# Kernel tuning notes

Measured on AMD Instinct MI355X. Metric: run time of the kernel, lower is better.

The kernel has to match this reference:

```python
import jax, jax.numpy as jnp
import numpy as np

B, N, CQ, CH, H = 2, 2048, 256, 256, 8
D = CH // H  # head_dim = 32


def setup_inputs() -> dict:
    key = jax.random.key(0)
    ks = jax.random.split(key, 10)
    s = 0.02
    return {
        "q_x": jax.random.normal(ks[0], (B, N, CQ), dtype=jnp.float32),
        "attn_bias": jax.random.normal(ks[1], (B, H, N, N), dtype=jnp.float32),
        "Wq": jax.random.normal(ks[2], (CQ, CH), dtype=jnp.float32) * s,
        "bq": jnp.zeros((CH,), dtype=jnp.float32),
        "Wk": jax.random.normal(ks[3], (CQ, CH), dtype=jnp.float32) * s,
        "Wv": jax.random.normal(ks[4], (CQ, CH), dtype=jnp.float32) * s,
        "Wout": jax.random.normal(ks[5], (CH, CQ), dtype=jnp.float32) * s,
        "bout": jnp.zeros((CQ,), dtype=jnp.float32),
        "Wg": jax.random.normal(ks[6], (CQ, CQ), dtype=jnp.float32) * s,
        "bg": jnp.zeros((CQ,), dtype=jnp.float32),
        "gbias": jnp.ones((CQ,), dtype=jnp.float32),
    }


def reference(q_x, attn_bias, Wq, bq, Wk, Wv, Wout, bout, Wg, bg, gbias):
    # prep_qkv: project, split heads; scale q by 1/sqrt(head_dim) (apply_scale path)
    scale = 1.0 / jnp.sqrt(jnp.asarray(D, q_x.dtype))
    q = ((q_x @ Wq + bq).reshape(B, N, H, D)) * scale  # [B,N,H,D]
    k = (q_x @ Wk).reshape(B, N, H, D)
    v = (q_x @ Wv).reshape(B, N, H, D)
    # attention with additive pair bias
    scores = jnp.einsum("bqhd,bkhd->bhqk", q, k) + attn_bias  # [B,H,N,N]
    attn = jax.nn.softmax(scores, axis=-1)
    o = jnp.einsum("bhqk,bkhd->bqhd", attn, v).reshape(B, N, CH)  # merge heads
    # wrap_up: output projection + sigmoid gate (gating_bias init ones)
    out = o @ Wout + bout  # [B,N,CQ]
    gate = jax.nn.sigmoid(q_x @ Wg + bg + gbias)
    return gate * out
```

## Files before the change

kernel.cpp:

```cpp
#include <hip/hip_runtime.h>

#define BB 2
#define NN 2048
#define CQc 256
#define CHc 256
#define HHc 8
#define DDc 32

typedef __bf16 bf16_t;
typedef bf16_t bf16x8 __attribute__((ext_vector_type(8)));
typedef float f32x4 __attribute__((ext_vector_type(4)));

#define LOG2E 1.4426950408889634f

static __device__ __forceinline__ unsigned short f2bf(float f) {
  union { float f; unsigned u; } a; a.f = f;
  unsigned r = a.u + 0x7FFFu + ((a.u >> 16) & 1u);
  return (unsigned short)(r >> 16);
}

static __device__ __forceinline__ bf16x8 ldb8(const unsigned short* p) {
  return *reinterpret_cast<const bf16x8*>(p);
}

__global__ void prep_w(const float* __restrict__ Wq, const float* __restrict__ Wk,
                       const float* __restrict__ Wv, const float* __restrict__ Wg,
                       const float* __restrict__ Wo, unsigned short* __restrict__ wt) {
  int gid = blockIdx.x * 256 + threadIdx.x;
  int w = gid >> 16, r = gid & 65535;
  int n = r >> 8, k = r & 255;
  const float* W = (w == 0) ? Wq : (w == 1) ? Wk : (w == 2) ? Wv : (w == 3) ? Wg : Wo;
  wt[gid] = f2bf(W[k * 256 + n]);
}

__global__ __launch_bounds__(256) void proj_k(
    const float* __restrict__ X, const float* __restrict__ bq,
    const float* __restrict__ bg, const float* __restrict__ gbias,
    const unsigned short* __restrict__ wt,
    unsigned short* __restrict__ q_ws, unsigned short* __restrict__ k_ws,
    unsigned short* __restrict__ vt_ws, float* __restrict__ gate_ws) {
  const int tid = threadIdx.x;
  const int wave = tid >> 6, l = tid & 63, g = l >> 4, l15 = l & 15;
  const int mrow = blockIdx.x * 64 + wave * 16 + l15;
  const int c0 = blockIdx.y * 64;
  const int widx = c0 >> 8;
  const int nin0 = c0 & 255;
  const unsigned short* W = wt + widx * 65536;

  f32x4 acc[4];
#pragma unroll
  for (int st = 0; st < 4; ++st) acc[st] = f32x4{0.f, 0.f, 0.f, 0.f};

#pragma unroll
  for (int kk0 = 0; kk0 < 256; kk0 += 32) {
    const float* xp = X + mrow * 256 + kk0 + 8 * g;
    f32x4 x0 = *reinterpret_cast<const f32x4*>(xp);
    f32x4 x1 = *reinterpret_cast<const f32x4*>(xp + 4);
    union { unsigned short u[8]; bf16x8 v; } av;
#pragma unroll
    for (int e = 0; e < 4; ++e) { av.u[e] = f2bf(x0[e]); av.u[4 + e] = f2bf(x1[e]); }
#pragma unroll
    for (int st = 0; st < 4; ++st) {
      bf16x8 bv = ldb8(W + (nin0 + st * 16 + l15) * 256 + kk0 + 8 * g);
      acc[st] = __builtin_amdgcn_mfma_f32_16x16x32_bf16(av.v, bv, acc[st], 0, 0, 0);
    }
  }

  const int mb = blockIdx.x * 64 + wave * 16 + 4 * g;
#pragma unroll
  for (int st = 0; st < 4; ++st) {
    const int n = nin0 + st * 16 + l15;
#pragma unroll
    for (int j = 0; j < 4; ++j) {
      const int m = mb + j;
      const int b = m >> 11, t = m & 2047;
      float val = acc[st][j];
      if (widx == 0) {
        int h = n >> 5, d = n & 31;
        q_ws[((b * 8 + h) * 2048 + t) * 32 + d] =
            f2bf((val + bq[n]) * (0.17677669529663687f * LOG2E));
      } else if (widx == 1) {
        int h = n >> 5, d = n & 31;
        k_ws[((b * 8 + h) * 2048 + t) * 32 + d] = f2bf(val);
      } else if (widx == 2) {
        int h = n >> 5, d = n & 31;
        vt_ws[((b * 8 + h) * 32 + d) * 2048 + t] = f2bf(val);
      } else {
        float z = val + bg[n] + gbias[n];
        gate_ws[m * 256 + n] = 1.0f / (1.0f + __expf(-z));
      }
    }
  }
}

__global__ __launch_bounds__(256) void attn_k(
    const unsigned short* __restrict__ q_ws, const unsigned short* __restrict__ k_ws,
    const unsigned short* __restrict__ vt_ws, const float* __restrict__ bias,
    unsigned short* __restrict__ o_ws) {
  __shared__ float sbias[4 * 3 * 1024];
  __shared__ unsigned short plds[4 * 16 * 72];
  const int tid = threadIdx.x;
  const int wave = tid >> 6, l = tid & 63, g = l >> 4, l15 = l & 15;
  const int bh = blockIdx.x >> 5, qt = blockIdx.x & 31;
  const int qr0 = qt * 64 + wave * 16;
  const int kvbase = bh * 2048;
  unsigned short* pw = plds + wave * (16 * 72);
  float* sb = sbias + wave * 3072;

  const bf16x8 qa = ldb8(q_ws + (size_t)(kvbase + qr0 + l15) * 32 + 8 * g);
  const unsigned short* kbase = k_ws + (size_t)kvbase * 32 + 8 * g + l15 * 32;
  const unsigned short* vbase = vt_ws + (size_t)(bh * 32 + l15) * 2048 + 8 * g;
  const float* bsrc = bias + ((size_t)bh << 22) + (size_t)(qr0 + (l >> 4)) * 2048 + (l & 15) * 4;

  auto stage = [&](int bidx, int k0) {
    float* dst = sb + bidx * 1024;
#pragma unroll
    for (int qq = 0; qq < 4; ++qq)
      __builtin_amdgcn_global_load_lds(
          (const __attribute__((address_space(1))) void*)(bsrc + (size_t)qq * 8192 + k0),
          (__attribute__((address_space(3))) void*)(dst + qq * 256), 16, 0, 0);
  };

  float mr[4], lr[4];
  f32x4 oacc[2];
#pragma unroll
  for (int j = 0; j < 4; ++j) { mr[j] = -1e30f; lr[j] = 0.0f; }
  oacc[0] = f32x4{0.f, 0.f, 0.f, 0.f};
  oacc[1] = f32x4{0.f, 0.f, 0.f, 0.f};

  stage(0, 0);
  stage(1, 64);
  int cb = 0;
#pragma unroll 1
  for (int kt = 0; kt < 32; ++kt) {
    const int k0 = kt * 64;
    if (kt < 31) {
      asm volatile("s_waitcnt vmcnt(4)" ::: "memory");
    } else {
      asm volatile("s_waitcnt vmcnt(0)" ::: "memory");
    }
    __builtin_amdgcn_sched_barrier(0);
    f32x4 cfr[4];
    const float* sbc = sb + cb * 1024 + l15;
#pragma unroll
    for (int st = 0; st < 4; ++st)
#pragma unroll
      for (int j = 0; j < 4; ++j)
        cfr[st][j] = sbc[(4 * g + j) * 64 + st * 16] * LOG2E;

    bf16x8 kb[4];
#pragma unroll
    for (int st = 0; st < 4; ++st) kb[st] = ldb8(kbase + (size_t)(k0 + st * 16) * 32);
    bf16x8 vb[2][2];
#pragma unroll
    for (int dst = 0; dst < 2; ++dst)
#pragma unroll
      for (int kc = 0; kc < 2; ++kc)
        vb[dst][kc] = ldb8(vbase + (size_t)dst * 16 * 2048 + k0 + kc * 32);

    int nb = cb + 2; if (nb >= 3) nb -= 3;
    if (kt < 30) stage(nb, k0 + 128);

    f32x4 s[4];
#pragma unroll
    for (int st = 0; st < 4; ++st)
      s[st] = __builtin_amdgcn_mfma_f32_16x16x32_bf16(qa, kb[st], cfr[st], 0, 0, 0);

#pragma unroll
    for (int j = 0; j < 4; ++j) {
      float mx = fmaxf(fmaxf(s[0][j], s[1][j]), fmaxf(s[2][j], s[3][j]));
      mx = fmaxf(mx, __shfl_xor(mx, 1));
      mx = fmaxf(mx, __shfl_xor(mx, 2));
      mx = fmaxf(mx, __shfl_xor(mx, 4));
      mx = fmaxf(mx, __shfl_xor(mx, 8));
      const float mn = fmaxf(mr[j], mx);
      const float sc = __builtin_amdgcn_exp2f(mr[j] - mn);
      mr[j] = mn;
      float rs = 0.f;
#pragma unroll
      for (int st = 0; st < 4; ++st) {
        float e = __builtin_amdgcn_exp2f(s[st][j] - mn);
        s[st][j] = e;
        rs += e;
      }
      rs += __shfl_xor(rs, 1);
      rs += __shfl_xor(rs, 2);
      rs += __shfl_xor(rs, 4);
      rs += __shfl_xor(rs, 8);
      lr[j] = lr[j] * sc + rs;
      oacc[0][j] *= sc;
      oacc[1][j] *= sc;
    }
#pragma unroll
    for (int st = 0; st < 4; ++st)
#pragma unroll
      for (int j = 0; j < 4; ++j)
        pw[(4 * g + j) * 72 + st * 16 + l15] = f2bf(s[st][j]);
#pragma unroll
    for (int kc = 0; kc < 2; ++kc) {
      bf16x8 pa = ldb8(pw + l15 * 72 + kc * 32 + 8 * g);
      oacc[0] = __builtin_amdgcn_mfma_f32_16x16x32_bf16(pa, vb[0][kc], oacc[0], 0, 0, 0);
      oacc[1] = __builtin_amdgcn_mfma_f32_16x16x32_bf16(pa, vb[1][kc], oacc[1], 0, 0, 0);
    }
    cb = cb + 1; if (cb >= 3) cb -= 3;
  }

  const int b = bh >> 3, h = bh & 7;
#pragma unroll
  for (int dst = 0; dst < 2; ++dst)
#pragma unroll
    for (int j = 0; j < 4; ++j) {
      const int q = qr0 + 4 * g + j;
      const float val = oacc[dst][j] / lr[j];
      o_ws[((size_t)(b * 2048 + q)) * 256 + h * 32 + dst * 16 + l15] = f2bf(val);
    }
}

__global__ __launch_bounds__(256) void outp_k(
    const unsigned short* __restrict__ o_ws, const unsigned short* __restrict__ wot,
    const float* __restrict__ bout, const float* __restrict__ gate_ws,
    float* __restrict__ out) {
  const int tid = threadIdx.x;
  const int wave = tid >> 6, l = tid & 63, g = l >> 4, l15 = l & 15;
  const int m0 = blockIdx.x * 64 + wave * 16;
  const int c0 = blockIdx.y * 64;
  f32x4 acc[4];
#pragma unroll
  for (int st = 0; st < 4; ++st) acc[st] = f32x4{0.f, 0.f, 0.f, 0.f};
#pragma unroll
  for (int kk0 = 0; kk0 < 256; kk0 += 32) {
    bf16x8 a = ldb8(o_ws + (m0 + l15) * 256 + kk0 + 8 * g);
#pragma unroll
    for (int st = 0; st < 4; ++st) {
      bf16x8 bv = ldb8(wot + (c0 + st * 16 + l15) * 256 + kk0 + 8 * g);
      acc[st] = __builtin_amdgcn_mfma_f32_16x16x32_bf16(a, bv, acc[st], 0, 0, 0);
    }
  }
  const int mb = m0 + 4 * g;
#pragma unroll
  for (int st = 0; st < 4; ++st) {
    const int n = c0 + st * 16 + l15;
#pragma unroll
    for (int j = 0; j < 4; ++j) {
      const int m = mb + j;
      const float val = acc[st][j] + bout[n];
      out[m * 256 + n] = gate_ws[m * 256 + n] * val;
    }
  }
}

extern "C" void kernel_launch(void* const* d_in, const int* in_sizes, int n_in,
                              void* d_out, int out_size, void* d_ws, size_t ws_size,
                              hipStream_t stream) {
  const float* q_x   = (const float*)d_in[0];
  const float* bias  = (const float*)d_in[1];
  const float* Wq    = (const float*)d_in[2];
  const float* bq    = (const float*)d_in[3];
  const float* Wk    = (const float*)d_in[4];
  const float* Wv    = (const float*)d_in[5];
  const float* Wout  = (const float*)d_in[6];
  const float* bout  = (const float*)d_in[7];
  const float* Wg    = (const float*)d_in[8];
  const float* bg    = (const float*)d_in[9];
  const float* gbias = (const float*)d_in[10];
  float* out = (float*)d_out;

  char* ws = (char*)d_ws;
  unsigned short* wt    = (unsigned short*)(ws);
  unsigned short* q_ws  = (unsigned short*)(ws + 655360);
  unsigned short* k_ws  = (unsigned short*)(ws + 655360 + 2097152);
  unsigned short* vt_ws = (unsigned short*)(ws + 655360 + 2 * 2097152);
  unsigned short* o_ws  = (unsigned short*)(ws + 655360 + 3 * 2097152);
  float* gate_ws        = (float*)(ws + 655360 + 4 * 2097152);

  prep_w<<<1280, 256, 0, stream>>>(Wq, Wk, Wv, Wg, Wout, wt);
  proj_k<<<dim3(64, 16), 256, 0, stream>>>(q_x, bq, bg, gbias, wt, q_ws, k_ws, vt_ws, gate_ws);
  attn_k<<<512, 256, 0, stream>>>(q_ws, k_ws, vt_ws, bias, o_ws);
  outp_k<<<dim3(64, 4), 256, 0, stream>>>(o_ws, wt + 4 * 65536, bout, gate_ws, out);
}
```

Baseline: 118.6 us.

## Split attention key range across waves with cross-wave softmax merge

Each block now handles 16 query rows instead of 64, and its four waves each process a different slice of keys. Partial max, sum and output are merged through shared memory at the end. The bias tile for each 512-key span is staged cooperatively into a double-buffered LDS array with block barriers. This quadruples the grid to give more parallelism and more bias loads in flight, at the cost of per-span barriers, a full vmcnt(0) drain, and an extra reduction epilogue. K and V loads are also no longer shared across waves.

```diff
diff --git a/kernel.cpp b/kernel.cpp
--- a/kernel.cpp
+++ b/kernel.cpp
@@ -97,29 +97,31 @@
     const unsigned short* __restrict__ q_ws, const unsigned short* __restrict__ k_ws,
     const unsigned short* __restrict__ vt_ws, const float* __restrict__ bias,
     unsigned short* __restrict__ o_ws) {
-  __shared__ float sbias[4 * 3 * 1024];
+  __shared__ float sbias[2][16][516];
   __shared__ unsigned short plds[4 * 16 * 72];
   const int tid = threadIdx.x;
   const int wave = tid >> 6, l = tid & 63, g = l >> 4, l15 = l & 15;
-  const int bh = blockIdx.x >> 5, qt = blockIdx.x & 31;
-  const int qr0 = qt * 64 + wave * 16;
+  const int bh = blockIdx.x >> 7, qt = blockIdx.x & 127;
+  const int qr0 = qt * 16;
   const int kvbase = bh * 2048;
   unsigned short* pw = plds + wave * (16 * 72);
-  float* sb = sbias + wave * 3072;
 
   const bf16x8 qa = ldb8(q_ws + (size_t)(kvbase + qr0 + l15) * 32 + 8 * g);
   const unsigned short* kbase = k_ws + (size_t)kvbase * 32 + 8 * g + l15 * 32;
   const unsigned short* vbase = vt_ws + (size_t)(bh * 32 + l15) * 2048 + 8 * g;
-  const float* bsrc = bias + ((size_t)bh << 22) + (size_t)(qr0 + (l >> 4)) * 2048 + (l & 15) * 4;
-
-  auto stage = [&](int bidx, int k0) {
-    float* dst = sb + bidx * 1024;
-#pragma unroll
-    for (int qq = 0; qq < 4; ++qq)
-      __builtin_amdgcn_global_load_lds(
-          (const __attribute__((address_space(1))) void*)(bsrc + (size_t)qq * 8192 + k0),
-          (__attribute__((address_space(3))) void*)(dst + qq * 256), 16, 0, 0);
-  };
+  const float* bias_base = bias + ((size_t)bh << 22) + (size_t)(qr0 + wave * 4) * 2048 + l * 4;
+
+#define STAGE(buf, sp, c)                                                          \
+  {                                                                                \
+    _Pragma("unroll") for (int rr = 2 * (c); rr < 2 * (c) + 2; ++rr)               \
+        _Pragma("unroll") for (int h = 0; h < 2; ++h)                              \
+            __builtin_amdgcn_global_load_lds(                                      \
+                (const __attribute__((address_space(1))) void*)(                   \
+                    bias_base + (size_t)rr * 2048 + (sp) * 512 + h * 256),         \
+                (__attribute__((address_space(3))) void*)(                         \
+                    &sbias[buf][wave * 4 + rr][h * 256]),                          \
+                16, 0, 0);                                                         \
+  }
 
   float mr[4], lr[4];
   f32x4 oacc[2];
@@ -128,92 +130,119 @@
   oacc[0] = f32x4{0.f, 0.f, 0.f, 0.f};
   oacc[1] = f32x4{0.f, 0.f, 0.f, 0.f};
 
-  stage(0, 0);
-  stage(1, 64);
-  int cb = 0;
+  STAGE(0, 0, 0);
+  STAGE(0, 0, 1);
+
 #pragma unroll 1
-  for (int kt = 0; kt < 32; ++kt) {
-    const int k0 = kt * 64;
-    if (kt < 31) {
-      asm volatile("s_waitcnt vmcnt(4)" ::: "memory");
-    } else {
-      asm volatile("s_waitcnt vmcnt(0)" ::: "memory");
-    }
+  for (int sp = 0; sp < 4; ++sp) {
+    const int buf = sp & 1;
+    asm volatile("s_waitcnt vmcnt(0)" ::: "memory");
+    __builtin_amdgcn_s_barrier();
     __builtin_amdgcn_sched_barrier(0);
-    f32x4 cfr[4];
-    const float* sbc = sb + cb * 1024 + l15;
-#pragma unroll
-    for (int st = 0; st < 4; ++st)
-#pragma unroll
-      for (int j = 0; j < 4; ++j)
-        cfr[st][j] = sbc[(4 * g + j) * 64 + st * 16] * LOG2E;
-
-    bf16x8 kb[4];
-#pragma unroll
-    for (int st = 0; st < 4; ++st) kb[st] = ldb8(kbase + (size_t)(k0 + st * 16) * 32);
-    bf16x8 vb[2][2];
-#pragma unroll
-    for (int dst = 0; dst < 2; ++dst)
-#pragma unroll
-      for (int kc = 0; kc < 2; ++kc)
-        vb[dst][kc] = ldb8(vbase + (size_t)dst * 16 * 2048 + k0 + kc * 32);
-
-    int nb = cb + 2; if (nb >= 3) nb -= 3;
-    if (kt < 30) stage(nb, k0 + 128);
-
-    f32x4 s[4];
-#pragma unroll
-    for (int st = 0; st < 4; ++st)
-      s[st] = __builtin_amdgcn_mfma_f32_16x16x32_bf16(qa, kb[st], cfr[st], 0, 0, 0);
-
+#pragma unroll
+    for (int t = 0; t < 2; ++t) {
+      const int tile = 2 * wave + t;
+      const int k0 = sp * 512 + tile * 64;
+      bf16x8 kb[4];
+#pragma unroll
+      for (int st = 0; st < 4; ++st) kb[st] = ldb8(kbase + (size_t)(k0 + st * 16) * 32);
+      bf16x8 vb[2][2];
+#pragma unroll
+      for (int dst = 0; dst < 2; ++dst)
+#pragma unroll
+        for (int kc = 0; kc < 2; ++kc)
+          vb[dst][kc] = ldb8(vbase + (size_t)dst * 16 * 2048 + k0 + kc * 32);
+      if (sp < 3) { STAGE(buf ^ 1, sp + 1, t); }
+      f32x4 cfr[4];
+#pragma unroll
+      for (int st = 0; st < 4; ++st)
+#pragma unroll
+        for (int j = 0; j < 4; ++j)
+          cfr[st][j] = sbias[buf][4 * g + j][tile * 64 + st * 16 + l15] * LOG2E;
+      f32x4 s[4];
+#pragma unroll
+      for (int st = 0; st < 4; ++st)
+        s[st] = __builtin_amdgcn_mfma_f32_16x16x32_bf16(qa, kb[st], cfr[st], 0, 0, 0);
+#pragma unroll
+      for (int j = 0; j < 4; ++j) {
+        float mx = fmaxf(fmaxf(s[0][j], s[1][j]), fmaxf(s[2][j], s[3][j]));
+        mx = fmaxf(mx, __shfl_xor(mx, 1));
+        mx = fmaxf(mx, __shfl_xor(mx, 2));
+        mx = fmaxf(mx, __shfl_xor(mx, 4));
+        mx = fmaxf(mx, __shfl_xor(mx, 8));
+        const float mn = fmaxf(mr[j], mx);
+        const float sc = __builtin_amdgcn_exp2f(mr[j] - mn);
+        mr[j] = mn;
+        float rs = 0.f;
+#pragma unroll
+        for (int st = 0; st < 4; ++st) {
+          float e = __builtin_amdgcn_exp2f(s[st][j] - mn);
+          s[st][j] = e;
+          rs += e;
+        }
+        rs += __shfl_xor(rs, 1);
+        rs += __shfl_xor(rs, 2);
+        rs += __shfl_xor(rs, 4);
+        rs += __shfl_xor(rs, 8);
+        lr[j] = lr[j] * sc + rs;
+        oacc[0][j] *= sc;
+        oacc[1][j] *= sc;
+      }
+#pragma unroll
+      for (int st = 0; st < 4; ++st)
+#pragma unroll
+        for (int j = 0; j < 4; ++j)
+          pw[(4 * g + j) * 72 + st * 16 + l15] = f2bf(s[st][j]);
+#pragma unroll
+      for (int kc = 0; kc < 2; ++kc) {
+        bf16x8 pa = ldb8(pw + l15 * 72 + kc * 32 + 8 * g);
+        oacc[0] = __builtin_amdgcn_mfma_f32_16x16x32_bf16(pa, vb[0][kc], oacc[0], 0, 0, 0);
+        oacc[1] = __builtin_amdgcn_mfma_f32_16x16x32_bf16(pa, vb[1][kc], oacc[1], 0, 0, 0);
+      }
+    }
+  }
+
+  float* obuf = (float*)sbias;
+  float* mlbuf = obuf + 4 * 16 * 32;
+  __syncthreads();
+#pragma unroll
+  for (int dst = 0; dst < 2; ++dst)
+#pragma unroll
+    for (int j = 0; j < 4; ++j)
+      obuf[wave * 512 + (4 * g + j) * 32 + dst * 16 + l15] = oacc[dst][j];
+  if (l15 == 0) {
 #pragma unroll
     for (int j = 0; j < 4; ++j) {
-      float mx = fmaxf(fmaxf(s[0][j], s[1][j]), fmaxf(s[2][j], s[3][j]));
-      mx = fmaxf(mx, __shfl_xor(mx, 1));
-      mx = fmaxf(mx, __shfl_xor(mx, 2));
-      mx = fmaxf(mx, __shfl_xor(mx, 4));
-      mx = fmaxf(mx, __shfl_xor(mx, 8));
-      const float mn = fmaxf(mr[j], mx);
-      const float sc = __builtin_amdgcn_exp2f(mr[j] - mn);
-      mr[j] = mn;
-      float rs = 0.f;
-#pragma unroll
-      for (int st = 0; st < 4; ++st) {
-        float e = __builtin_amdgcn_exp2f(s[st][j] - mn);
-        s[st][j] = e;
-        rs += e;
+      mlbuf[wave * 32 + (4 * g + j) * 2 + 0] = mr[j];
+      mlbuf[wave * 32 + (4 * g + j) * 2 + 1] = lr[j];
+    }
+  }
+  __syncthreads();
+  if (wave == 0) {
+    const int b = bh >> 3, h = bh & 7;
+#pragma unroll
+    for (int j = 0; j < 4; ++j) {
+      const int r = 4 * g + j;
+      float m0 = mlbuf[r * 2], m1 = mlbuf[32 + r * 2];
+      float m2 = mlbuf[64 + r * 2], m3 = mlbuf[96 + r * 2];
+      const float ms = fmaxf(fmaxf(m0, m1), fmaxf(m2, m3));
+      const float w0 = __builtin_amdgcn_exp2f(m0 - ms);
+      const float w1 = __builtin_amdgcn_exp2f(m1 - ms);
+      const float w2 = __builtin_amdgcn_exp2f(m2 - ms);
+      const float w3 = __builtin_amdgcn_exp2f(m3 - ms);
+      const float den = mlbuf[r * 2 + 1] * w0 + mlbuf[32 + r * 2 + 1] * w1 +
+                        mlbuf[64 + r * 2 + 1] * w2 + mlbuf[96 + r * 2 + 1] * w3;
+      const int q = qr0 + r;
+#pragma unroll
+      for (int dst = 0; dst < 2; ++dst) {
+        const int c = dst * 16 + l15;
+        const float num = obuf[r * 32 + c] * w0 + obuf[512 + r * 32 + c] * w1 +
+                          obuf[1024 + r * 32 + c] * w2 + obuf[1536 + r * 32 + c] * w3;
+        o_ws[((size_t)(b * 2048 + q)) * 256 + h * 32 + c] = f2bf(num / den);
       }
-      rs += __shfl_xor(rs, 1);
-      rs += __shfl_xor(rs, 2);
-      rs += __shfl_xor(rs, 4);
-      rs += __shfl_xor(rs, 8);
-      lr[j] = lr[j] * sc + rs;
-      oacc[0][j] *= sc;
-      oacc[1][j] *= sc;
-    }
-#pragma unroll
-    for (int st = 0; st < 4; ++st)
-#pragma unroll
-      for (int j = 0; j < 4; ++j)
-        pw[(4 * g + j) * 72 + st * 16 + l15] = f2bf(s[st][j]);
-#pragma unroll
-    for (int kc = 0; kc < 2; ++kc) {
-      bf16x8 pa = ldb8(pw + l15 * 72 + kc * 32 + 8 * g);
-      oacc[0] = __builtin_amdgcn_mfma_f32_16x16x32_bf16(pa, vb[0][kc], oacc[0], 0, 0, 0);
-      oacc[1] = __builtin_amdgcn_mfma_f32_16x16x32_bf16(pa, vb[1][kc], oacc[1], 0, 0, 0);
-    }
-    cb = cb + 1; if (cb >= 3) cb -= 3;
-  }
-
-  const int b = bh >> 3, h = bh & 7;
-#pragma unroll
-  for (int dst = 0; dst < 2; ++dst)
-#pragma unroll
-    for (int j = 0; j < 4; ++j) {
-      const int q = qr0 + 4 * g + j;
-      const float val = oacc[dst][j] / lr[j];
-      o_ws[((size_t)(b * 2048 + q)) * 256 + h * 32 + dst * 16 + l15] = f2bf(val);
-    }
+    }
+  }
+#undef STAGE
 }
 
 __global__ __launch_bounds__(256) void outp_k(
@@ -275,6 +304,6 @@
 
   prep_w<<<1280, 256, 0, stream>>>(Wq, Wk, Wv, Wg, Wout, wt);
   proj_k<<<dim3(64, 16), 256, 0, stream>>>(q_x, bq, bg, gbias, wt, q_ws, k_ws, vt_ws, gate_ws);
-  attn_k<<<512, 256, 0, stream>>>(q_ws, k_ws, vt_ws, bias, o_ws);
+  attn_k<<<2048, 256, 0, stream>>>(q_ws, k_ws, vt_ws, bias, o_ws);
   outp_k<<<dim3(64, 4), 256, 0, stream>>>(o_ws, wt + 4 * 65536, bout, gate_ws, out);
 }
```

Result: slower. 131.3 us (+10.7%).

## Fuse gate GEMM into output projection, pre-convert X to bf16, tile V transpose

Applied to the files above, without the earlier changes.

Weight prep now transposes through shared-memory tiles and also converts q_x to bf16 once, so the projection kernels read bf16 activations instead of converting fp32 per block. The gate projection moves from proj_k into outp_k, which computes both the Wout and Wg GEMMs and applies the sigmoid inline, removing the fp32 gate buffer write and read. The V transpose store is staged through LDS so vt_ws gets coalesced 16-byte writes. In exchange outp_k does twice the MFMA work and carries more registers.

```diff
diff --git a/kernel.cpp b/kernel.cpp
--- a/kernel.cpp
+++ b/kernel.cpp
@@ -1,15 +1,9 @@
 #include <hip/hip_runtime.h>
-
-#define BB 2
-#define NN 2048
-#define CQc 256
-#define CHc 256
-#define HHc 8
-#define DDc 32
 
 typedef __bf16 bf16_t;
 typedef bf16_t bf16x8 __attribute__((ext_vector_type(8)));
 typedef float f32x4 __attribute__((ext_vector_type(4)));
+typedef unsigned short ushort8 __attribute__((ext_vector_type(8)));
 
 #define LOG2E 1.4426950408889634f
 
@@ -23,28 +17,45 @@
   return *reinterpret_cast<const bf16x8*>(p);
 }
 
-__global__ void prep_w(const float* __restrict__ Wq, const float* __restrict__ Wk,
-                       const float* __restrict__ Wv, const float* __restrict__ Wg,
-                       const float* __restrict__ Wo, unsigned short* __restrict__ wt) {
-  int gid = blockIdx.x * 256 + threadIdx.x;
-  int w = gid >> 16, r = gid & 65535;
-  int n = r >> 8, k = r & 255;
-  const float* W = (w == 0) ? Wq : (w == 1) ? Wk : (w == 2) ? Wv : (w == 3) ? Wg : Wo;
-  wt[gid] = f2bf(W[k * 256 + n]);
+__global__ __launch_bounds__(256) void prep_k(
+    const float* __restrict__ Wq, const float* __restrict__ Wk,
+    const float* __restrict__ Wv, const float* __restrict__ Wg,
+    const float* __restrict__ Wo, const float* __restrict__ X,
+    unsigned short* __restrict__ wt, unsigned short* __restrict__ xb) {
+  const int bid = blockIdx.x;
+  if (bid < 320) {
+    __shared__ float t[32][33];
+    const int w = bid >> 6, tile = bid & 63;
+    const int r0 = (tile >> 3) * 32, c0 = (tile & 7) * 32;
+    const float* W = (w == 0) ? Wq : (w == 1) ? Wk : (w == 2) ? Wv : (w == 3) ? Wg : Wo;
+    const int x = threadIdx.x & 31, y = threadIdx.x >> 5;
+#pragma unroll
+    for (int yy = 0; yy < 32; yy += 8) t[y + yy][x] = W[(r0 + y + yy) * 256 + c0 + x];
+    __syncthreads();
+#pragma unroll
+    for (int yy = 0; yy < 32; yy += 8)
+      wt[w * 65536 + (c0 + y + yy) * 256 + r0 + x] = f2bf(t[x][y + yy]);
+  } else {
+    const int i = (bid - 320) * 1024 + threadIdx.x * 4;
+    const f32x4 v = *reinterpret_cast<const f32x4*>(X + i);
+    unsigned short o[4];
+#pragma unroll
+    for (int e = 0; e < 4; ++e) o[e] = f2bf(v[e]);
+    *reinterpret_cast<unsigned long long*>(xb + i) = *reinterpret_cast<unsigned long long*>(o);
+  }
 }
 
 __global__ __launch_bounds__(256) void proj_k(
-    const float* __restrict__ X, const float* __restrict__ bq,
-    const float* __restrict__ bg, const float* __restrict__ gbias,
+    const unsigned short* __restrict__ xb, const float* __restrict__ bq,
     const unsigned short* __restrict__ wt,
     unsigned short* __restrict__ q_ws, unsigned short* __restrict__ k_ws,
-    unsigned short* __restrict__ vt_ws, float* __restrict__ gate_ws) {
+    unsigned short* __restrict__ vt_ws) {
+  __shared__ unsigned short vtile[64][72];
   const int tid = threadIdx.x;
   const int wave = tid >> 6, l = tid & 63, g = l >> 4, l15 = l & 15;
   const int mrow = blockIdx.x * 64 + wave * 16 + l15;
-  const int c0 = blockIdx.y * 64;
-  const int widx = c0 >> 8;
-  const int nin0 = c0 & 255;
+  const int widx = blockIdx.y >> 2;
+  const int nin0 = (blockIdx.y & 3) * 64;
   const unsigned short* W = wt + widx * 65536;
 
   f32x4 acc[4];
@@ -53,41 +64,46 @@
 
 #pragma unroll
   for (int kk0 = 0; kk0 < 256; kk0 += 32) {
-    const float* xp = X + mrow * 256 + kk0 + 8 * g;
-    f32x4 x0 = *reinterpret_cast<const f32x4*>(xp);
-    f32x4 x1 = *reinterpret_cast<const f32x4*>(xp + 4);
-    union { unsigned short u[8]; bf16x8 v; } av;
-#pragma unroll
-    for (int e = 0; e < 4; ++e) { av.u[e] = f2bf(x0[e]); av.u[4 + e] = f2bf(x1[e]); }
+    const bf16x8 av = ldb8(xb + mrow * 256 + kk0 + 8 * g);
 #pragma unroll
     for (int st = 0; st < 4; ++st) {
       bf16x8 bv = ldb8(W + (nin0 + st * 16 + l15) * 256 + kk0 + 8 * g);
-      acc[st] = __builtin_amdgcn_mfma_f32_16x16x32_bf16(av.v, bv, acc[st], 0, 0, 0);
+      acc[st] = __builtin_amdgcn_mfma_f32_16x16x32_bf16(av, bv, acc[st], 0, 0, 0);
     }
   }
 
   const int mb = blockIdx.x * 64 + wave * 16 + 4 * g;
-#pragma unroll
-  for (int st = 0; st < 4; ++st) {
-    const int n = nin0 + st * 16 + l15;
-#pragma unroll
-    for (int j = 0; j < 4; ++j) {
-      const int m = mb + j;
-      const int b = m >> 11, t = m & 2047;
-      float val = acc[st][j];
-      if (widx == 0) {
-        int h = n >> 5, d = n & 31;
-        q_ws[((b * 8 + h) * 2048 + t) * 32 + d] =
-            f2bf((val + bq[n]) * (0.17677669529663687f * LOG2E));
-      } else if (widx == 1) {
-        int h = n >> 5, d = n & 31;
-        k_ws[((b * 8 + h) * 2048 + t) * 32 + d] = f2bf(val);
-      } else if (widx == 2) {
-        int h = n >> 5, d = n & 31;
-        vt_ws[((b * 8 + h) * 32 + d) * 2048 + t] = f2bf(val);
-      } else {
-        float z = val + bg[n] + gbias[n];
-        gate_ws[m * 256 + n] = 1.0f / (1.0f + __expf(-z));
+  if (widx == 2) {
+#pragma unroll
+    for (int st = 0; st < 4; ++st)
+#pragma unroll
+      for (int j = 0; j < 4; ++j)
+        vtile[st * 16 + l15][wave * 16 + 4 * g + j] = f2bf(acc[st][j]);
+    __syncthreads();
+    const int b = (blockIdx.x * 64) >> 11;
+    const int t0 = (blockIdx.x * 64) & 2047;
+#pragma unroll
+    for (int it = tid; it < 512; it += 256) {
+      const int r = it >> 3, cseg = (it & 7) * 8;
+      const int n = nin0 + r;
+      *reinterpret_cast<ushort8*>(vt_ws + (size_t)((b * 8 + (n >> 5)) * 32 + (n & 31)) * 2048 +
+                                  t0 + cseg) = *reinterpret_cast<const ushort8*>(&vtile[r][cseg]);
+    }
+  } else {
+#pragma unroll
+    for (int st = 0; st < 4; ++st) {
+      const int n = nin0 + st * 16 + l15;
+      const int h = n >> 5, d = n & 31;
+#pragma unroll
+      for (int j = 0; j < 4; ++j) {
+        const int m = mb + j;
+        const int b = m >> 11, t = m & 2047;
+        if (widx == 0) {
+          q_ws[((b * 8 + h) * 2048 + t) * 32 + d] =
+              f2bf((acc[st][j] + bq[n]) * (0.17677669529663687f * LOG2E));
+        } else {
+          k_ws[((b * 8 + h) * 2048 + t) * 32 + d] = f2bf(acc[st][j]);
+        }
       }
     }
   }
@@ -217,23 +233,32 @@
 }
 
 __global__ __launch_bounds__(256) void outp_k(
-    const unsigned short* __restrict__ o_ws, const unsigned short* __restrict__ wot,
-    const float* __restrict__ bout, const float* __restrict__ gate_ws,
+    const unsigned short* __restrict__ o_ws, const unsigned short* __restrict__ wt,
+    const unsigned short* __restrict__ xb, const float* __restrict__ bout,
+    const float* __restrict__ bg, const float* __restrict__ gbias,
     float* __restrict__ out) {
   const int tid = threadIdx.x;
   const int wave = tid >> 6, l = tid & 63, g = l >> 4, l15 = l & 15;
   const int m0 = blockIdx.x * 64 + wave * 16;
   const int c0 = blockIdx.y * 64;
-  f32x4 acc[4];
-#pragma unroll
-  for (int st = 0; st < 4; ++st) acc[st] = f32x4{0.f, 0.f, 0.f, 0.f};
+  const unsigned short* wgt = wt + 3 * 65536;
+  const unsigned short* wot = wt + 4 * 65536;
+  f32x4 acco[4], accg[4];
+#pragma unroll
+  for (int st = 0; st < 4; ++st) {
+    acco[st] = f32x4{0.f, 0.f, 0.f, 0.f};
+    accg[st] = f32x4{0.f, 0.f, 0.f, 0.f};
+  }
 #pragma unroll
   for (int kk0 = 0; kk0 < 256; kk0 += 32) {
-    bf16x8 a = ldb8(o_ws + (m0 + l15) * 256 + kk0 + 8 * g);
+    const bf16x8 a_o = ldb8(o_ws + (m0 + l15) * 256 + kk0 + 8 * g);
+    const bf16x8 a_x = ldb8(xb + (m0 + l15) * 256 + kk0 + 8 * g);
 #pragma unroll
     for (int st = 0; st < 4; ++st) {
-      bf16x8 bv = ldb8(wot + (c0 + st * 16 + l15) * 256 + kk0 + 8 * g);
-      acc[st] = __builtin_amdgcn_mfma_f32_16x16x32_bf16(a, bv, acc[st], 0, 0, 0);
+      bf16x8 bo = ldb8(wot + (c0 + st * 16 + l15) * 256 + kk0 + 8 * g);
+      acco[st] = __builtin_amdgcn_mfma_f32_16x16x32_bf16(a_o, bo, acco[st], 0, 0, 0);
+      bf16x8 bgf = ldb8(wgt + (c0 + st * 16 + l15) * 256 + kk0 + 8 * g);
+      accg[st] = __builtin_amdgcn_mfma_f32_16x16x32_bf16(a_x, bgf, accg[st], 0, 0, 0);
     }
   }
   const int mb = m0 + 4 * g;
@@ -243,8 +268,9 @@
 #pragma unroll
     for (int j = 0; j < 4; ++j) {
       const int m = mb + j;
-      const float val = acc[st][j] + bout[n];
-      out[m * 256 + n] = gate_ws[m * 256 + n] * val;
+      const float z = accg[st][j] + bg[n] + gbias[n];
+      const float gate = 1.0f / (1.0f + __expf(-z));
+      out[m * 256 + n] = gate * (acco[st][j] + bout[n]);
     }
   }
 }
@@ -267,14 +293,14 @@
 
   char* ws = (char*)d_ws;
   unsigned short* wt    = (unsigned short*)(ws);
-  unsigned short* q_ws  = (unsigned short*)(ws + 655360);
-  unsigned short* k_ws  = (unsigned short*)(ws + 655360 + 2097152);
-  unsigned short* vt_ws = (unsigned short*)(ws + 655360 + 2 * 2097152);
-  unsigned short* o_ws  = (unsigned short*)(ws + 655360 + 3 * 2097152);
-  float* gate_ws        = (float*)(ws + 655360 + 4 * 2097152);
-
-  prep_w<<<1280, 256, 0, stream>>>(Wq, Wk, Wv, Wg, Wout, wt);
-  proj_k<<<dim3(64, 16), 256, 0, stream>>>(q_x, bq, bg, gbias, wt, q_ws, k_ws, vt_ws, gate_ws);
+  unsigned short* xb    = (unsigned short*)(ws + 655360);
+  unsigned short* q_ws  = (unsigned short*)(ws + 655360 + 2097152);
+  unsigned short* k_ws  = (unsigned short*)(ws + 655360 + 2 * 2097152);
+  unsigned short* vt_ws = (unsigned short*)(ws + 655360 + 3 * 2097152);
+  unsigned short* o_ws  = (unsigned short*)(ws + 655360 + 4 * 2097152);
+
+  prep_k<<<1344, 256, 0, stream>>>(Wq, Wk, Wv, Wg, Wout, q_x, wt, xb);
+  proj_k<<<dim3(64, 12), 256, 0, stream>>>(xb, bq, wt, q_ws, k_ws, vt_ws);
   attn_k<<<512, 256, 0, stream>>>(q_ws, k_ws, vt_ws, bias, o_ws);
-  outp_k<<<dim3(64, 4), 256, 0, stream>>>(o_ws, wt + 4 * 65536, bout, gate_ws, out);
-}
+  outp_k<<<dim3(64, 4), 256, 0, stream>>>(o_ws, wt, xb, bout, bg, gbias, out);
+}
```

Result: faster. 112.0 us (-5.6%).
